# Performance work log

Measured on AMD Instinct MI355X. Metric: run time of the kernel, lower is better.

The kernel has to match this reference:

```python
import jax, jax.numpy as jnp
import numpy as np

EPS = 1e-7
FEAT_DIM = 128
N_DATA = 100000
NCE_K = 16384
NCE_T = 0.07


def _l2norm(x):
    # Normalize(power=2): x / (sum(x^2, axis=1)^(1/2))
    return x / jnp.sqrt(jnp.sum(x * x, axis=1, keepdims=True))


def _embed(x, W, b):
    return _l2norm(x @ W.T + b)


def _contrast_loss(x, n_data):
    # x: [B, K+1] of (unnormalized) probabilities; col 0 = positive
    bsz = x.shape[0]
    m = x.shape[1] - 1
    Pn = 1.0 / float(n_data)
    c = m * Pn + EPS
    log_D1 = jnp.log(x[:, 0] / (x[:, 0] + c))          # positives
    log_D0 = jnp.log((m * Pn) / (x[:, 1:] + c))         # negatives
    return -(log_D1.sum() + log_D0.sum()) / bsz


def setup_inputs() -> dict:
    key = jax.random.key(0)
    ks = jax.random.split(key, 10)
    s_dim, t_dim = 1024, 2048
    B = 64
    stdv = 1.0 / np.sqrt(FEAT_DIM / 3.0)
    inp = {
        "f_s": jax.random.normal(ks[0], (B, s_dim), dtype=jnp.float32),
        "f_t": jax.random.normal(ks[1], (B, t_dim), dtype=jnp.float32),
        "idx": jax.random.randint(ks[2], (B,), 0, N_DATA),
        "contrast_idx": jax.random.randint(ks[3], (B, NCE_K + 1), 0, N_DATA),
        # Embed params (linear): Linear(dim_in, feat_dim)
        "Ws": jax.random.normal(ks[4], (FEAT_DIM, s_dim), dtype=jnp.float32) / np.sqrt(s_dim),
        "bs": jnp.zeros((FEAT_DIM,), dtype=jnp.float32),
        "Wt": jax.random.normal(ks[5], (FEAT_DIM, t_dim), dtype=jnp.float32) / np.sqrt(t_dim),
        "bt": jnp.zeros((FEAT_DIM,), dtype=jnp.float32),
        # memory banks, init uniform(-stdv, stdv) as in CRD ContrastMemory
        "memory_v1": jax.random.uniform(ks[6], (N_DATA, FEAT_DIM), jnp.float32, -stdv, stdv),
        "memory_v2": jax.random.uniform(ks[7], (N_DATA, FEAT_DIM), jnp.float32, -stdv, stdv),
    }
    return inp


def reference(f_s, f_t, idx, contrast_idx, Ws, bs, Wt, bt, memory_v1, memory_v2):
    v_s = _embed(f_s, Ws, bs)   # [B, D]
    v_t = _embed(f_t, Wt, bt)   # [B, D]

    # idx.select(1,0).copy_(y): column 0 is the positive index
    idx_all = jnp.concatenate([idx[:, None], contrast_idx[:, 1:]], axis=1)  # [B, K+1]

    # gather from memory banks + bmm similarity
    w1 = memory_v1[idx_all]   # [B, K+1, D] (v_t side bank)
    w2 = memory_v2[idx_all]   # [B, K+1, D] (v_s side bank)
    out_t = jnp.exp(jnp.einsum('bkd,bd->bk', w1, v_t) / NCE_T)  # out_v2
    out_s = jnp.exp(jnp.einsum('bkd,bd->bk', w2, v_s) / NCE_T)  # out_v1

    # Z set on first batch: Z = out.mean() * n_data (detached constant)
    Z_s = jax.lax.stop_gradient(out_s.mean()) * N_DATA
    Z_t = jax.lax.stop_gradient(out_t.mean()) * N_DATA
    out_s = out_s / Z_s
    out_t = out_t / Z_t

    s_loss = _contrast_loss(out_s, N_DATA)
    t_loss = _contrast_loss(out_t, N_DATA)
    return s_loss + t_loss
```

## Files before the change

### kernel.cpp

```cpp
#include <hip/hip_runtime.h>

#define NDATA 100000
#define KP1 16385
#define BSZ 64
#define PTOT (BSZ * KP1)
#define NCHUNKS 6250
#define INV_T (1.0f / 0.07f)
#define ACC_STRIDE 64
#define ACC_GROUPS 32
#define SG_NW 2048
#define HSEG 12500

typedef short short8 __attribute__((ext_vector_type(8)));
typedef float f32x4 __attribute__((ext_vector_type(4)));

__device__ __forceinline__ float wave_reduce64(float v) {
    #pragma unroll
    for (int off = 32; off >= 1; off >>= 1) v += __shfl_xor(v, off);
    return v;
}

__device__ __forceinline__ float group_reduce16(float v) {
    v += __shfl_xor(v, 8); v += __shfl_xor(v, 4);
    v += __shfl_xor(v, 2); v += __shfl_xor(v, 1);
    return v;
}

__device__ __forceinline__ unsigned short f2bf(float f) {
    unsigned u = __float_as_uint(f);
    u += 0x7FFFu + ((u >> 16) & 1u);
    return (unsigned short)(u >> 16);
}

__device__ __forceinline__ float bfm(float x) {
    return __uint_as_float(((unsigned)f2bf(x)) << 16);
}

__device__ __forceinline__ short8 pack_bf16(float4 lo, float4 hi) {
    short8 r;
    r[0] = (short)f2bf(lo.x); r[1] = (short)f2bf(lo.y);
    r[2] = (short)f2bf(lo.z); r[3] = (short)f2bf(lo.w);
    r[4] = (short)f2bf(hi.x); r[5] = (short)f2bf(hi.y);
    r[6] = (short)f2bf(hi.z); r[7] = (short)f2bf(hi.w);
    return r;
}

__device__ __forceinline__ float dot4(float4 a, float4 b, float acc) {
    acc = fmaf(a.x, b.x, acc);
    acc = fmaf(a.y, b.y, acc);
    acc = fmaf(a.z, b.z, acc);
    return fmaf(a.w, b.w, acc);
}

__device__ __forceinline__ float dot8bf(const float4* a, const float4* v, int li, float d) {
    #pragma unroll
    for (int h = 0; h < 2; ++h) {
        const float4 x = a[li * 2 + h], y = v[li * 2 + h];
        d = fmaf(bfm(x.x), bfm(y.x), d);
        d = fmaf(bfm(x.y), bfm(y.y), d);
        d = fmaf(bfm(x.z), bfm(y.z), d);
        d = fmaf(bfm(x.w), bfm(y.w), d);
    }
    return d;
}

__global__ __launch_bounds__(256) void embedhist_kernel(
    const float* __restrict__ fs, const float* __restrict__ ft,
    const float* __restrict__ Ws, const float* __restrict__ bs,
    const float* __restrict__ Wt, const float* __restrict__ bt,
    const int* __restrict__ cidx,
    float* __restrict__ vraw_s, float* __restrict__ vraw_t,
    float* __restrict__ n2part, unsigned* __restrict__ cntw,
    float* __restrict__ acc)
{
    const int t = threadIdx.x;
    __shared__ __align__(16) unsigned char smem[50048];

    if (blockIdx.x < 128) {
        unsigned* h = (unsigned*)smem;
        const int w   = blockIdx.x >> 3;
        const int seg = blockIdx.x & 7;
        const int r0  = seg * HSEG;

        for (int i = t; i < HSEG; i += 256) h[i] = 0;
        __syncthreads();

        #pragma unroll
        for (int j2 = 0; j2 < 4; ++j2) {
            const int b = 4 * w + j2;
            const unsigned inc = 1u << (8 * j2);
            const int* __restrict__ cp = cidx + (size_t)b * KP1 + 1;
            for (int bi = 0; bi < 8; ++bi) {
                int v[8];
                #pragma unroll
                for (int u = 0; u < 8; ++u)
                    v[u] = cp[bi * 2048 + u * 256 + t];
                #pragma unroll
                for (int u = 0; u < 8; ++u) {
                    const unsigned rr = (unsigned)(v[u] - r0);
                    if (rr < HSEG) atomicAdd(&h[rr], inc);
                }
            }
        }
        __syncthreads();

        unsigned* __restrict__ dstp = cntw + (size_t)w * NDATA + r0;
        for (int i = t; i < HSEG; i += 256) dstp[i] = h[i];
        return;
    }

    const int bx = blockIdx.x - 128;
    if (bx < 8) acc[bx * 256 + t] = 0.0f;

    float4* FS = (float4*)smem;
    float4* FT = (float4*)(smem + 8192);
    float*  NR = (float*)(smem + 24576);

    const int dq = bx >> 5;
    const int b0 = (bx & 31) * 2;

    for (int q = t; q < 512; q += 256) {
        const int b = q >> 8, i = q & 255;
        FS[q] = ((const float4*)(fs + (size_t)(b0 + b) * 1024))[i];
    }
    for (int q = t; q < 1024; q += 256) {
        const int b = q >> 9, i = q & 511;
        FT[q] = ((const float4*)(ft + (size_t)(b0 + b) * 2048))[i];
    }
    __syncthreads();

    const int w = t >> 6, lane = t & 63;
    const int d = dq * 4 + w;

    {
        const float4* wrow = (const float4*)(Ws + (size_t)d * 1024);
        float a0 = 0.0f, a1 = 0.0f;
        #pragma unroll
        for (int i = 0; i < 4; ++i) {
            const float4 wv = wrow[i * 64 + lane];
            a0 = dot4(wv, FS[i * 64 + lane], a0);
            a1 = dot4(wv, FS[256 + i * 64 + lane], a1);
        }
        a0 = wave_reduce64(a0) + bs[d];
        a1 = wave_reduce64(a1) + bs[d];
        if (lane == 0) {
            vraw_s[(size_t)b0 * 128 + d]       = a0;
            vraw_s[(size_t)(b0 + 1) * 128 + d] = a1;
            NR[w * 4 + 0] = a0 * a0;
            NR[w * 4 + 1] = a1 * a1;
        }
    }
    {
        const float4* wrow = (const float4*)(Wt + (size_t)d * 2048);
        float a0 = 0.0f, a1 = 0.0f;
        #pragma unroll
        for (int i = 0; i < 8; ++i) {
            const float4 wv = wrow[i * 64 + lane];
            a0 = dot4(wv, FT[i * 64 + lane], a0);
            a1 = dot4(wv, FT[512 + i * 64 + lane], a1);
        }
        a0 = wave_reduce64(a0) + bt[d];
        a1 = wave_reduce64(a1) + bt[d];
        if (lane == 0) {
            vraw_t[(size_t)b0 * 128 + d]       = a0;
            vraw_t[(size_t)(b0 + 1) * 128 + d] = a1;
            NR[w * 4 + 2] = a0 * a0;
            NR[w * 4 + 3] = a1 * a1;
        }
    }
    __syncthreads();
    if (t < 4) {
        const float v = NR[0 * 4 + t] + NR[1 * 4 + t] + NR[2 * 4 + t] + NR[3 * 4 + t];
        const int side = (t < 2) ? 1 : 0;
        const int bb = b0 + (t & 1);
        n2part[side * 2048 + bb * 32 + dq] = v;
    }
}

#define SG_ISSUE(AB, CB, CID)                                                \
  {                                                                          \
    const int r0_ = (CID) << 4;                                              \
    const float4* ar_ = (const float4*)(bankp + (size_t)(r0_ + m) * 128);    \
    _Pragma("unroll")                                                        \
    for (int kk = 0; kk < 4; ++kk) {                                         \
      AB[kk * 2]     = ar_[(kk * 4 + q4) * 2];                               \
      AB[kk * 2 + 1] = ar_[(kk * 4 + q4) * 2 + 1];                           \
    }                                                                        \
    _Pragma("unroll")                                                        \
    for (int n = 0; n < 4; ++n)                                              \
      CB[n] = cntw[(size_t)(n * 4 + q4) * NDATA + (r0_ + m)];                \
  }

#define SG_PROCESS(AB, CB)                                                   \
  {                                                                          \
    short8 af_[4];                                                           \
    _Pragma("unroll")                                                        \
    for (int kk = 0; kk < 4; ++kk)                                           \
      af_[kk] = pack_bf16(AB[kk * 2], AB[kk * 2 + 1]);                       \
    _Pragma("unroll")                                                        \
    for (int n = 0; n < 4; ++n) {                                            \
      f32x4 av = {0.f, 0.f, 0.f, 0.f};                                       \
      _Pragma("unroll")                                                      \
      for (int kk = 0; kk < 4; ++kk)                                         \
        av = __builtin_amdgcn_mfma_f32_16x16x32_bf16(bfv[n][kk], af_[kk], av, 0, 0, 0); \
      const unsigned cw_ = CB[n];                                            \
      _Pragma("unroll")                                                      \
      for (int j = 0; j < 4; ++j) {                                          \
        const float fm_ = (float)((cw_ >> (8 * j)) & 255u);                  \
        const float e_  = __expf(av[j] * scv[n][j]);                         \
        se  = fmaf(e_, fm_, se);                                             \
        se2 = fmaf(e_ * fm_, e_, se2);                                       \
      }                                                                      \
    }                                                                        \
  }

__global__ __launch_bounds__(256) void sgemm_kernel(
    const float* __restrict__ m1, const float* __restrict__ m2,
    const float* __restrict__ vraw_s, const float* __restrict__ vraw_t,
    const float* __restrict__ n2part,
    const unsigned* __restrict__ cntw,
    float* __restrict__ acc)
{
    const int t = threadIdx.x;
    const int bank = blockIdx.y;
    const float* __restrict__ bankp = bank ? m2 : m1;
    const float* __restrict__ vp    = bank ? vraw_s : vraw_t;

    __shared__ float scl[64];
    {
        const int tb = t >> 2, tg = t & 3;
        const float* np = n2part + bank * 2048 + tb * 32 + tg * 8;
        float s = 0.0f;
        #pragma unroll
        for (int j = 0; j < 8; ++j) s += np[j];
        s += __shfl_xor(s, 1);
        s += __shfl_xor(s, 2);
        if (tg == 0) scl[tb] = INV_T * rsqrtf(s);
    }
    __syncthreads();

    const int lane = t & 63;
    const int m  = lane & 15;
    const int q4 = lane >> 4;

    short8 bfv[4][4];
    #pragma unroll
    for (int n = 0; n < 4; ++n) {
        const float4* vrow = (const float4*)(vp + (size_t)(n * 16 + m) * 128);
        #pragma unroll
        for (int kk = 0; kk < 4; ++kk) {
            const float4 lo = vrow[(kk * 4 + q4) * 2];
            const float4 hi = vrow[(kk * 4 + q4) * 2 + 1];
            bfv[n][kk] = pack_bf16(lo, hi);
        }
    }

    f32x4 scv[4];
    #pragma unroll
    for (int n = 0; n < 4; ++n) {
        #pragma unroll
        for (int j = 0; j < 4; ++j) scv[n][j] = scl[n * 16 + q4 * 4 + j];
    }

    float se = 0.0f, se2 = 0.0f;

    const int wave = (blockIdx.x << 2) | (t >> 6);

    float4 aA[8], aB[8];
    unsigned cA[4], cB[4];

    SG_ISSUE(aA, cA, wave);
    SG_ISSUE(aB, cB, wave + SG_NW);
    SG_PROCESS(aA, cA);
    SG_ISSUE(aA, cA, wave + 2 * SG_NW);
    SG_PROCESS(aB, cB);
    if (wave + 3 * SG_NW < NCHUNKS) {
        SG_ISSUE(aB, cB, wave + 3 * SG_NW);
        SG_PROCESS(aA, cA);
        SG_PROCESS(aB, cB);
    } else {
        SG_PROCESS(aA, cA);
    }

    se  = wave_reduce64(se);
    se2 = wave_reduce64(se2);
    __shared__ float red[4][2];
    if (lane == 0) { red[t >> 6][0] = se; red[t >> 6][1] = se2; }
    __syncthreads();
    if (t < 2) {
        const float s = red[0][t] + red[1][t] + red[2][t] + red[3][t];
        atomicAdd(&acc[(blockIdx.x & (ACC_GROUPS - 1)) * ACC_STRIDE + bank * 2 + t], s);
    }
}

__global__ __launch_bounds__(256) void final_kernel(
    const int* __restrict__ idx,
    const float* __restrict__ m1, const float* __restrict__ m2,
    const float* __restrict__ vraw_t, const float* __restrict__ vraw_s,
    const float* __restrict__ n2part,
    const float* __restrict__ acc, float* __restrict__ out)
{
    const int t = threadIdx.x, wave = t >> 6, lane = t & 63, g = lane >> 4, li = lane & 15;
    __shared__ float sctl[64], scsl[64];
    __shared__ float e1s[64], e2s[64];

    if (t < 128) {
        const int side = t >> 6, b = t & 63;
        const float* np = n2part + side * 2048 + b * 32;
        float s = 0.0f;
        for (int j = 0; j < 32; ++j) s += np[j];
        (side ? scsl : sctl)[b] = INV_T * rsqrtf(s);
    }
    __syncthreads();

    #pragma unroll
    for (int i = 0; i < 4; ++i) {
        const int b = wave * 16 + i * 4 + g;
        const int row = idx[b];
        float dT = dot8bf((const float4*)(m1 + (size_t)row * 128),
                          (const float4*)(vraw_t + (size_t)b * 128), li, 0.f);
        float dS = dot8bf((const float4*)(m2 + (size_t)row * 128),
                          (const float4*)(vraw_s + (size_t)b * 128), li, 0.f);
        dT = group_reduce16(dT);
        dS = group_reduce16(dS);
        if (li == 0) {
            e1s[b] = __expf(dT * sctl[b]);
            e2s[b] = __expf(dS * scsl[b]);
        }
    }
    __syncthreads();

    if (t < 64) {
        const int b = t;
        const float c = 0.16384f + 1e-7f;
        const float e1p = e1s[b], e2p = e2s[b];

        const float pseT = wave_reduce64(e1p);
        const float pseS = wave_reduce64(e2p);

        float seT_neg = 0.f, se2T_neg = 0.f, seS_neg = 0.f, se2S_neg = 0.f;
        for (int s = 0; s < ACC_GROUPS; ++s) {
            seT_neg  += acc[s * ACC_STRIDE + 0];
            se2T_neg += acc[s * ACC_STRIDE + 1];
            seS_neg  += acc[s * ACC_STRIDE + 2];
            se2S_neg += acc[s * ACC_STRIDE + 3];
        }

        const float zn = (float)PTOT / (float)NDATA;
        const float invZt = zn / (seT_neg + pseT);
        const float invZs = zn / (seS_neg + pseS);

        const float PB = (float)(PTOT - BSZ);
        const float LOG_MPN_C = -6.1035156e-7f;
        const float ic = 1.0f / c;

        const float negT = PB * LOG_MPN_C
                         - seT_neg * invZt * ic
                         + 0.5f * se2T_neg * invZt * invZt * ic * ic;
        const float negS = PB * LOG_MPN_C
                         - seS_neg * invZs * ic
                         + 0.5f * se2S_neg * invZs * invZs * ic * ic;

        const float x0t = e1p * invZt, x0s = e2p * invZs;
        float pos = __logf(x0t / (x0t + c)) + __logf(x0s / (x0s + c));
        pos = wave_reduce64(pos);

        if (b == 0) out[0] = -(negT + negS + pos) * (1.0f / 64.0f);
    }
}

extern "C" void kernel_launch(void* const* d_in, const int* in_sizes, int n_in,
                              void* d_out, int out_size, void* d_ws, size_t ws_size,
                              hipStream_t stream) {
    const float* fs   = (const float*)d_in[0];
    const float* ft   = (const float*)d_in[1];
    const int*   idx  = (const int*)d_in[2];
    const int*   cidx = (const int*)d_in[3];
    const float* Ws   = (const float*)d_in[4];
    const float* bs   = (const float*)d_in[5];
    const float* Wt   = (const float*)d_in[6];
    const float* bt   = (const float*)d_in[7];
    const float* m1   = (const float*)d_in[8];
    const float* m2   = (const float*)d_in[9];
    float* out = (float*)d_out;

    float* ws      = (float*)d_ws;
    float* acc     = ws;
    float* n2part  = ws + 2048;
    unsigned* cntw = (unsigned*)(ws + 8192);
    float* vraw_s  = ws + 1608192;
    float* vraw_t  = ws + 1616384;

    embedhist_kernel<<<dim3(1152), dim3(256), 0, stream>>>(
        fs, ft, Ws, bs, Wt, bt, cidx, vraw_s, vraw_t, n2part, cntw, acc);
    sgemm_kernel<<<dim3(512, 2), dim3(256), 0, stream>>>(
        m1, m2, vraw_s, vraw_t, n2part, cntw, acc);
    final_kernel<<<dim3(1), dim3(256), 0, stream>>>(
        idx, m1, m2, vraw_t, vraw_s, n2part, acc, out);
}
```

Baseline: 186.3 us.

## Move bf16 query fragments to swizzled LDS and raise sgemm occupancy

The bf16-packed query vectors, previously held per-thread in registers, now live in a shared-memory tile with XOR-swizzled addresses. The per-lane scale registers are replaced by direct shared-memory reads. The explicit double-buffered issue/process pipeline is dropped in favour of a simpler one- or two-chunk loop, and the grid is widened to 782 blocks with a minimum-occupancy hint of 5. The goal is to cut VGPR pressure so more waves can hide memory-bank gather latency, at the cost of extra LDS reads per MFMA and losing the explicit prefetch overlap.

```diff
diff --git a/kernel.cpp b/kernel.cpp
--- a/kernel.cpp
+++ b/kernel.cpp
@@ -8,7 +8,8 @@
 #define INV_T (1.0f / 0.07f)
 #define ACC_STRIDE 64
 #define ACC_GROUPS 32
-#define SG_NW 2048
+#define SG_NW 3128
+#define SG_TAIL 3122
 #define HSEG 12500
 
 typedef short short8 __attribute__((ext_vector_type(8)));
@@ -177,44 +178,45 @@
     }
 }
 
-#define SG_ISSUE(AB, CB, CID)                                                \
+#define SGP(CID)                                                             \
   {                                                                          \
     const int r0_ = (CID) << 4;                                              \
     const float4* ar_ = (const float4*)(bankp + (size_t)(r0_ + m) * 128);    \
+    float4 a_[8];                                                            \
     _Pragma("unroll")                                                        \
     for (int kk = 0; kk < 4; ++kk) {                                         \
-      AB[kk * 2]     = ar_[(kk * 4 + q4) * 2];                               \
-      AB[kk * 2 + 1] = ar_[(kk * 4 + q4) * 2 + 1];                           \
+      a_[kk * 2]     = ar_[(kk * 4 + q4) * 2];                               \
+      a_[kk * 2 + 1] = ar_[(kk * 4 + q4) * 2 + 1];                           \
     }                                                                        \
+    unsigned c_[4];                                                          \
     _Pragma("unroll")                                                        \
     for (int n = 0; n < 4; ++n)                                              \
-      CB[n] = cntw[(size_t)(n * 4 + q4) * NDATA + (r0_ + m)];                \
-  }
-
-#define SG_PROCESS(AB, CB)                                                   \
-  {                                                                          \
+      c_[n] = cntw[(size_t)(n * 4 + q4) * NDATA + (r0_ + m)];                \
     short8 af_[4];                                                           \
     _Pragma("unroll")                                                        \
     for (int kk = 0; kk < 4; ++kk)                                           \
-      af_[kk] = pack_bf16(AB[kk * 2], AB[kk * 2 + 1]);                       \
+      af_[kk] = pack_bf16(a_[kk * 2], a_[kk * 2 + 1]);                       \
     _Pragma("unroll")                                                        \
     for (int n = 0; n < 4; ++n) {                                            \
       f32x4 av = {0.f, 0.f, 0.f, 0.f};                                       \
       _Pragma("unroll")                                                      \
-      for (int kk = 0; kk < 4; ++kk)                                         \
-        av = __builtin_amdgcn_mfma_f32_16x16x32_bf16(bfv[n][kk], af_[kk], av, 0, 0, 0); \
-      const unsigned cw_ = CB[n];                                            \
+      for (int kk = 0; kk < 4; ++kk) {                                       \
+        const int row_ = n * 16 + m;                                         \
+        const short8 bv = *(const short8*)&Vb[((row_ * 128 + (kk * 4 + q4) * 8) ^ ((m & 7) << 3))]; \
+        av = __builtin_amdgcn_mfma_f32_16x16x32_bf16(bv, af_[kk], av, 0, 0, 0); \
+      }                                                                      \
+      const unsigned cw_ = c_[n];                                            \
       _Pragma("unroll")                                                      \
       for (int j = 0; j < 4; ++j) {                                          \
         const float fm_ = (float)((cw_ >> (8 * j)) & 255u);                  \
-        const float e_  = __expf(av[j] * scv[n][j]);                         \
+        const float e_  = __expf(av[j] * scl[n * 16 + q4 * 4 + j]);          \
         se  = fmaf(e_, fm_, se);                                             \
         se2 = fmaf(e_ * fm_, e_, se2);                                       \
       }                                                                      \
     }                                                                        \
   }
 
-__global__ __launch_bounds__(256) void sgemm_kernel(
+__global__ __launch_bounds__(256, 5) void sgemm_kernel(
     const float* __restrict__ m1, const float* __restrict__ m2,
     const float* __restrict__ vraw_s, const float* __restrict__ vraw_t,
     const float* __restrict__ n2part,
@@ -226,7 +228,22 @@
     const float* __restrict__ bankp = bank ? m2 : m1;
     const float* __restrict__ vp    = bank ? vraw_s : vraw_t;
 
+    __shared__ __align__(16) unsigned short Vb[8192];
     __shared__ float scl[64];
+    __shared__ float red[4][2];
+
+    {
+        const int r = t >> 2;
+        const int s0 = (t & 3) * 4;
+        const float4* vr = (const float4*)(vp + (size_t)r * 128);
+        #pragma unroll
+        for (int q = 0; q < 4; ++q) {
+            const int s = s0 + q;
+            const float4 lo = vr[s * 2];
+            const float4 hi = vr[s * 2 + 1];
+            *(short8*)&Vb[((r * 128 + s * 8) ^ ((r & 7) << 3))] = pack_bf16(lo, hi);
+        }
+    }
     {
         const int tb = t >> 2, tg = t & 3;
         const float* np = n2part + bank * 2048 + tb * 32 + tg * 8;
@@ -243,48 +260,17 @@
     const int m  = lane & 15;
     const int q4 = lane >> 4;
 
-    short8 bfv[4][4];
-    #pragma unroll
-    for (int n = 0; n < 4; ++n) {
-        const float4* vrow = (const float4*)(vp + (size_t)(n * 16 + m) * 128);
-        #pragma unroll
-        for (int kk = 0; kk < 4; ++kk) {
-            const float4 lo = vrow[(kk * 4 + q4) * 2];
-            const float4 hi = vrow[(kk * 4 + q4) * 2 + 1];
-            bfv[n][kk] = pack_bf16(lo, hi);
-        }
-    }
-
-    f32x4 scv[4];
-    #pragma unroll
-    for (int n = 0; n < 4; ++n) {
-        #pragma unroll
-        for (int j = 0; j < 4; ++j) scv[n][j] = scl[n * 16 + q4 * 4 + j];
-    }
-
     float se = 0.0f, se2 = 0.0f;
 
     const int wave = (blockIdx.x << 2) | (t >> 6);
 
-    float4 aA[8], aB[8];
-    unsigned cA[4], cB[4];
-
-    SG_ISSUE(aA, cA, wave);
-    SG_ISSUE(aB, cB, wave + SG_NW);
-    SG_PROCESS(aA, cA);
-    SG_ISSUE(aA, cA, wave + 2 * SG_NW);
-    SG_PROCESS(aB, cB);
-    if (wave + 3 * SG_NW < NCHUNKS) {
-        SG_ISSUE(aB, cB, wave + 3 * SG_NW);
-        SG_PROCESS(aA, cA);
-        SG_PROCESS(aB, cB);
-    } else {
-        SG_PROCESS(aA, cA);
+    SGP(wave);
+    if (wave < SG_TAIL) {
+        SGP(wave + SG_NW);
     }
 
     se  = wave_reduce64(se);
     se2 = wave_reduce64(se2);
-    __shared__ float red[4][2];
     if (lane == 0) { red[t >> 6][0] = se; red[t >> 6][1] = se2; }
     __syncthreads();
     if (t < 2) {
@@ -393,7 +379,7 @@
 
     embedhist_kernel<<<dim3(1152), dim3(256), 0, stream>>>(
         fs, ft, Ws, bs, Wt, bt, cidx, vraw_s, vraw_t, n2part, cntw, acc);
-    sgemm_kernel<<<dim3(512, 2), dim3(256), 0, stream>>>(
+    sgemm_kernel<<<dim3(782, 2), dim3(256), 0, stream>>>(
         m1, m2, vraw_s, vraw_t, n2part, cntw, acc);
     final_kernel<<<dim3(1), dim3(256), 0, stream>>>(
         idx, m1, m2, vraw_t, vraw_s, n2part, acc, out);
```

Result: slower. 205.4 us (+10.3%).
